# Optimization experiments

Measured on AMD Instinct MI355X. Metric: run time of the kernel, lower is better.

## Reference

```python
import jax, jax.numpy as jnp
import numpy as np

T, B, N, KALL, F, ORD, DIN, H, NH, HD, DE, DOUT = 4, 4, 16384, 4, 16384, 3, 4, 64, 4, 16, 4, 64


def setup_inputs() -> dict:
    key = jax.random.key(0)
    ks = jax.random.split(key, 32)
    p = lambda k, shape: (jax.random.normal(k, shape) * 0.1).astype(jnp.float32)
    indices = jax.random.randint(ks[0], (F, ORD), 0, N, dtype=jnp.int32)
    cnt = jnp.zeros((N,), jnp.float32).at[indices.reshape(-1)].add(1.0)
    nnz = jnp.maximum(cnt, 1.0)  # per-node nonzero count (avoid div-by-zero)
    return {
        "h": p(ks[1], (B, N, H)),
        "h_global": p(ks[2], (B, KALL, DOUT)),
        "x": p(ks[3], (T, B, N, DIN)),
        "extra": p(ks[4], (T, B, KALL, DE)),
        "dones": jax.random.bernoulli(ks[5], 0.1, (T, B)),
        "indices": indices,
        "nnz": nnz,
        # GRU cell params (flax GRUCell layout: i-dense with bias, h-dense no bias except n-gate)
        "Wi": p(ks[6], (DIN, 3 * H)), "bi": p(ks[7], (3 * H,)),
        "Wh": p(ks[8], (H, 3 * H)), "bhn": p(ks[9], (H,)),
        # MultiHeadAttention params
        "Wq": p(ks[10], (H, NH, HD)), "bq": p(ks[11], (NH, HD)),
        "Wk": p(ks[12], (H, NH, HD)), "bk": p(ks[13], (NH, HD)),
        "Wv": p(ks[14], (H, NH, HD)), "bv": p(ks[15], (NH, HD)),
        "Wo": p(ks[16], (NH, HD, H)), "bo": p(ks[17], (H,)),
        # output MLP (logit head) and value head
        "W1": p(ks[18], (H + DE, DOUT)), "b1": p(ks[19], (DOUT,)),
        "W2": p(ks[20], (DOUT, 1)), "b2": p(ks[21], (1,)),
        "Wv1": p(ks[22], (H + DE, 1)), "bv1": p(ks[23], (1,)),
    }


def reference(h, h_global, x, extra, dones, indices, nnz,
              Wi, bi, Wh, bhn, Wq, bq, Wk, bk, Wv, bv, Wo, bo,
              W1, b1, W2, b2, Wv1, bv1):
    Hd = Wh.shape[0]

    def gru_step(carry, inp):
        xt, dt = inp  # xt: [B,N,din], dt: [B]
        c = jnp.where(dt[:, None, None], jnp.zeros_like(carry), carry)
        gi = xt @ Wi + bi          # [B,N,3H]
        gh = c @ Wh                # [B,N,3H]
        r = jax.nn.sigmoid(gi[..., :Hd] + gh[..., :Hd])
        z = jax.nn.sigmoid(gi[..., Hd:2 * Hd] + gh[..., Hd:2 * Hd])
        n = jnp.tanh(gi[..., 2 * Hd:] + r * (gh[..., 2 * Hd:] + bhn))
        new = (1.0 - z) * n + z * c
        return new, new

    h_fin, hs = jax.lax.scan(gru_step, h, (x, dones))  # hs: [T,B,N,H]

    # gather per-factor neighbor hidden states
    g = jnp.take(hs, indices, axis=2)  # [T,B,F,ord,H]
    q = jnp.einsum('tbfkh,hnd->tbfknd', g, Wq) + bq
    kk = jnp.einsum('tbfkh,hnd->tbfknd', g, Wk) + bk
    vv = jnp.einsum('tbfkh,hnd->tbfknd', g, Wv) + bv
    scale = 1.0 / np.sqrt(q.shape[-1]).astype(np.float32)
    att = jax.nn.softmax(jnp.einsum('tbfqnd,tbfknd->tbfnqk', q * scale, kk), axis=-1)
    o = jnp.einsum('tbfnqk,tbfknd->tbfqnd', att, vv)
    a = jnp.einsum('tbfknd,ndh->tbfkh', o, Wo) + bo  # [T,B,F,ord,H]

    Tn, Bn = a.shape[0], a.shape[1]
    Nn = nnz.shape[0]
    a_flat = a.reshape(Tn, Bn, -1, a.shape[-1])  # [T,B,F*ord,H]
    # segment-sum scatter back to nodes, normalized by nnz
    y = jnp.zeros((Tn, Bn, Nn, a.shape[-1]), a.dtype).at[:, :, indices.reshape(-1), :].add(a_flat)
    y = y / nnz[None, None, :, None]

    Kall = extra.shape[2]
    N0 = Nn // Kall
    ypi = y.reshape(Tn, Bn, Kall, N0, y.shape[-1])
    y_global = jnp.mean(ypi, axis=3)                       # [T,B,K,H]
    z_global = jnp.concatenate((y_global, extra), axis=3)  # [T,B,K,H+DE]
    extra_t = jnp.broadcast_to(extra[:, :, :, None, :], (Tn, Bn, Kall, N0, extra.shape[-1]))
    z = jnp.concatenate((ypi, extra_t), axis=4).reshape(Tn, Bn, Nn, -1)
    value = (z_global @ Wv1 + bv1).sum(axis=2)             # [T,B,1]
    logit = (jax.nn.relu(z @ W1 + b1) @ W2 + b2).squeeze(axis=3)  # [T,B,N]
    return h_fin, h_global, logit, value.squeeze(axis=-1)
```

## Files before the change

kernel.cpp:

```cpp
#include <hip/hip_runtime.h>
#include <hip/hip_bf16.h>

#define T_ 4
#define B_ 4
#define N_ 16384
#define KALL_ 4
#define F_ 16384
#define ORD_ 3
#define DIN_ 4
#define H_ 64
#define H3_ 192
#define DE_ 4
#define STR 72
#define NE_ 49152

typedef __attribute__((ext_vector_type(8))) short s16x8;
typedef __attribute__((ext_vector_type(4))) float f32x4;
typedef unsigned long long u64;

static __device__ __forceinline__ float b2f(unsigned short u) {
  union { unsigned u; float f; } x; x.u = ((unsigned)u) << 16; return x.f;
}
static __device__ __forceinline__ unsigned short f2b(float f) {
  __hip_bfloat16 h = __float2bfloat16(f);
  union { __hip_bfloat16 h; unsigned short u; } x; x.h = h; return x.u;
}
static __device__ __forceinline__ float sigm_fast(float v) {
  return __builtin_amdgcn_rcpf(1.f + __expf(-v));
}
static __device__ __forceinline__ float tanh_fast(float v) {
  float e = __expf(2.f * v);
  return 1.f - 2.f * __builtin_amdgcn_rcpf(e + 1.f);
}

__global__ __launch_bounds__(256) void k_csr_count(
    const int* __restrict__ idx, int* __restrict__ cnt) {
  int e = blockIdx.x * 256 + threadIdx.x;
  if (e < NE_) atomicAdd(&cnt[idx[e]], 1);
}
__global__ __launch_bounds__(256) void k_csr_scan(
    const int* __restrict__ cnt, int* __restrict__ offs, int* __restrict__ cursor) {
  __shared__ int part[256];
  __shared__ int base[256];
  int t = threadIdx.x;
  int s = 0;
  for (int j = 0; j < 64; ++j) s += cnt[t * 64 + j];
  part[t] = s;
  __syncthreads();
  if (t == 0) {
    int run = 0;
    for (int i = 0; i < 256; ++i) { base[i] = run; run += part[i]; }
  }
  __syncthreads();
  int run = base[t];
  for (int j = 0; j < 64; ++j) {
    offs[t * 64 + j] = run;
    cursor[t * 64 + j] = run;
    run += cnt[t * 64 + j];
  }
  if (t == 255) offs[N_] = run;
}
__global__ __launch_bounds__(256) void k_csr_fill(
    const int* __restrict__ idx, int* __restrict__ cursor, int* __restrict__ elist) {
  int e = blockIdx.x * 256 + threadIdx.x;
  if (e < NE_) {
    int pos = atomicAdd(&cursor[idx[e]], 1);
    elist[pos] = e;
  }
}

__global__ __launch_bounds__(256) void k_prep_wh(
    const float* __restrict__ Wh, unsigned short* __restrict__ whTg) {
  int i = blockIdx.x * 256 + threadIdx.x;
  int rr = i >> 6, k = i & 63;
  int ct = rr >> 4, c = rr & 15;
  int g = ct >> 2, cg = ct & 3;
  whTg[i] = f2b(Wh[k * H3_ + g * 64 + 4 * c + cg]);
}

__global__ __launch_bounds__(256) void k_gru(
    const float* __restrict__ h0,
    const float* __restrict__ x,
    const int* __restrict__ dones,
    const unsigned short* __restrict__ whTg,
    const float* __restrict__ Wi,
    const float* __restrict__ bi,
    const float* __restrict__ bhn,
    unsigned short* __restrict__ hs,
    float* __restrict__ hfin)
{
  __shared__ __align__(16) short whT[H3_ * 72];
  __shared__ __align__(16) short carry[H_ * 72];
  __shared__ float wiS[5 * H3_];

  const int tid = threadIdx.x;
  const int lane = tid & 63;
  const int w = tid >> 6;
  const int c15 = lane & 15;
  const int hi4 = lane >> 4;
  const int bid = blockIdx.x;
  const int b = bid >> 8;
  const int nbase = (bid & 255) * 64;
  const int hb = 4 * c15;

#pragma unroll
  for (int c = 0; c < 6; ++c) {
    int lin = (c * 256 + tid) * 8;
    int row = lin >> 6, col = lin & 63;
    *(s16x8*)&whT[row * 72 + col] = *(const s16x8*)&whTg[lin];
  }
  for (int i = tid; i < 5 * H3_; i += 256)
    wiS[i] = (i < 4 * H3_) ? Wi[i] : bi[i - 4 * H3_];

  f32x4 cf[4];
#pragma unroll
  for (int r = 0; r < 4; ++r) {
    int row = 16 * w + 4 * hi4 + r;
    cf[r] = *(const f32x4*)&h0[(size_t)(b * N_ + nbase + row) * H_ + hb];
    u64 pk = 0;
#pragma unroll
    for (int e = 0; e < 4; ++e) pk |= (u64)f2b(cf[r][e]) << (16 * e);
    *(u64*)&carry[row * 72 + hb] = pk;
  }

  float bhnr[4];
#pragma unroll
  for (int cg = 0; cg < 4; ++cg) bhnr[cg] = bhn[hb + cg];

  unsigned dmask = 0;
  {
    bool word = true;
#pragma unroll
    for (int i = 0; i < 16; ++i) {
      int v = dones[i];
      if (v != 0 && v != 1 && v != 0x3F800000) word = false;
    }
#pragma unroll
    for (int t = 0; t < T_; ++t) {
      int tb = t * B_ + b;
      bool d = word ? (dones[tb] != 0) : (((const unsigned char*)dones)[tb] != 0);
      if (d) dmask |= (1u << t);
    }
  }

  __syncthreads();

  const int rowA = 16 * w + c15;
  for (int t = 0; t < T_; ++t) {
    if ((dmask >> t) & 1u) {
#pragma unroll
      for (int r = 0; r < 4; ++r) {
        cf[r] = (f32x4){0.f, 0.f, 0.f, 0.f};
        *(u64*)&carry[(16 * w + 4 * hi4 + r) * 72 + hb] = 0ull;
      }
    }

    f32x4 acc[12];
#pragma unroll
    for (int ct = 0; ct < 12; ++ct) acc[ct] = (f32x4){0.f, 0.f, 0.f, 0.f};
#pragma unroll
    for (int ks = 0; ks < 2; ++ks) {
      const int kb = ks * 32 + hi4 * 8;
      s16x8 af = *(const s16x8*)&carry[rowA * 72 + kb];
#pragma unroll
      for (int ct = 0; ct < 12; ++ct) {
        s16x8 bfr = *(const s16x8*)&whT[(16 * ct + c15) * 72 + kb];
        acc[ct] = __builtin_amdgcn_mfma_f32_16x16x32_bf16(af, bfr, acc[ct], 0, 0, 0);
      }
    }

#pragma unroll
    for (int r = 0; r < 4; ++r) {
      const int row = 16 * w + 4 * hi4 + r;
      const int node = nbase + row;
      const f32x4 xv = *(const f32x4*)&x[(size_t)((t * B_ + b) * N_ + node) * DIN_];
      f32x4 gi[3];
#pragma unroll
      for (int g = 0; g < 3; ++g) {
        f32x4 s = *(const f32x4*)&wiS[4 * H3_ + g * 64 + hb];
#pragma unroll
        for (int kk = 0; kk < 4; ++kk) {
          f32x4 wv = *(const f32x4*)&wiS[kk * H3_ + g * 64 + hb];
          s += xv[kk] * wv;
        }
        gi[g] = s;
      }
      f32x4 nc4;
      u64 pk = 0;
#pragma unroll
      for (int cg = 0; cg < 4; ++cg) {
        float rg = sigm_fast(gi[0][cg] + acc[cg][r]);
        float zg = sigm_fast(gi[1][cg] + acc[4 + cg][r]);
        float ng = tanh_fast(gi[2][cg] + rg * (acc[8 + cg][r] + bhnr[cg]));
        float nc = zg * (cf[r][cg] - ng) + ng;
        nc4[cg] = nc;
        pk |= (u64)f2b(nc) << (16 * cg);
      }
      cf[r] = nc4;
      *(u64*)&hs[(size_t)((t * B_ + b) * N_ + node) * H_ + hb] = pk;
      *(u64*)&carry[row * 72 + hb] = pk;
      if (t == T_ - 1)
        *(f32x4*)&hfin[(size_t)(b * N_ + node) * H_ + hb] = nc4;
    }
  }
}

__global__ __launch_bounds__(256, 3) void k_attn(
    const int tb0,
    const unsigned short* __restrict__ hs,
    const int* __restrict__ indices,
    const float* __restrict__ Wq, const float* __restrict__ bq,
    const float* __restrict__ Wk, const float* __restrict__ bk,
    const float* __restrict__ Wv, const float* __restrict__ bv,
    const float* __restrict__ Wo, const float* __restrict__ bo,
    unsigned short* __restrict__ a_edge)
{
  __shared__ __align__(16) unsigned short bufrag[3072];
  __shared__ __align__(8)  unsigned short qkvs[9792];
  __shared__ float biasf[4][64];
  __shared__ int idxs[48];

  const int tid = threadIdx.x;
  const int lane = tid & 63;
  const int w = tid >> 6;
  const int c15 = lane & 15;
  const int hi4 = lane >> 4;
  const int bid = blockIdx.x;
  const int col = 16 * w + c15;
  const int swz = (c15 ^ (hi4 << 2));

  if (tid < 48) idxs[tid] = indices[bid * 48 + tid];
  if (tid < 64) {
    biasf[0][tid] = bq[tid];
    biasf[1][tid] = bk[tid];
    biasf[2][tid] = bv[tid];
    biasf[3][tid] = bo[tid];
  }

  s16x8 wB[3][2], wB3[2];
#pragma unroll
  for (int m = 0; m < 3; ++m) {
    const float* Wm = (m == 0) ? Wq : (m == 1) ? Wk : Wv;
#pragma unroll
    for (int ks = 0; ks < 2; ++ks) {
      union { s16x8 v; short s[8]; } u;
#pragma unroll
      for (int j = 0; j < 8; ++j)
        u.s[j] = (short)f2b(Wm[(ks * 32 + hi4 * 8 + j) * 64 + col]);
      wB[m][ks] = u.v;
    }
  }
#pragma unroll
  for (int ks = 0; ks < 2; ++ks) {
    union { s16x8 v; short s[8]; } u;
#pragma unroll
    for (int j = 0; j < 8; ++j)
      u.s[j] = (short)f2b(Wo[(ks * 32 + hi4 * 8 + j) * 64 + col]);
    wB3[ks] = u.v;
  }
  __syncthreads();

  u64 pf[3];
#pragma unroll
  for (int k = 0; k < 3; ++k) {
    int idx = k * 256 + tid, row = idx >> 4, g = idx & 15;
    pf[k] = *(const u64*)&hs[((size_t)tb0 * N_ + idxs[row]) * H_ + g * 4];
  }

  for (int it = 0; it < 8; ++it) {
    __syncthreads();
#pragma unroll
    for (int k = 0; k < 3; ++k) {
      int idx = k * 256 + tid, row = idx >> 4, g = idx & 15;
      int rt = row >> 4, cr = row & 15;
      int ks = g >> 3, h5 = (g >> 1) & 3, j = (g & 1) * 4;
      int cr2 = cr ^ (h5 << 2);
      *(u64*)&bufrag[((rt * 2 + ks) << 9) + ((h5 * 16 + cr2) << 3) + j] = pf[k];
    }
    __syncthreads();

    s16x8 afr[3][2];
#pragma unroll
    for (int rt = 0; rt < 3; ++rt)
#pragma unroll
      for (int ks = 0; ks < 2; ++ks)
        afr[rt][ks] = *(const s16x8*)&bufrag[((rt * 2 + ks) << 9) + ((hi4 * 16 + swz) << 3)];
#pragma unroll
    for (int m = 0; m < 3; ++m) {
      float bias = biasf[m][col];
      float scl = (m == 0) ? 0.25f : 1.f;
#pragma unroll
      for (int rt = 0; rt < 3; ++rt) {
        f32x4 acc = (f32x4){0.f, 0.f, 0.f, 0.f};
        acc = __builtin_amdgcn_mfma_f32_16x16x32_bf16(afr[rt][0], wB[m][0], acc, 0, 0, 0);
        acc = __builtin_amdgcn_mfma_f32_16x16x32_bf16(afr[rt][1], wB[m][1], acc, 0, 0, 0);
#pragma unroll
        for (int r = 0; r < 4; ++r) {
          int row = 16 * rt + hi4 * 4 + r;
          qkvs[m * 3264 + row * 68 + col] = f2b((acc[r] + bias) * scl);
        }
      }
    }
    if (it < 7) {
      const size_t base = (size_t)(tb0 + it + 1) * N_;
#pragma unroll
      for (int k = 0; k < 3; ++k) {
        int idx = k * 256 + tid, row = idx >> 4, g = idx & 15;
        pf[k] = *(const u64*)&hs[(base + idxs[row]) * H_ + g * 4];
      }
    }
    __syncthreads();

    {
      int f = tid >> 4, head = (tid >> 2) & 3, dq = tid & 3;
      int colb = head * 16 + dq * 4;
      float qv[3][4], kv[3][4], vv[3][4];
#pragma unroll
      for (int qi = 0; qi < 3; ++qi) {
        int base = (3 * f + qi) * 68 + colb;
        u64 uq = *(const u64*)&qkvs[base];
        u64 uk = *(const u64*)&qkvs[3264 + base];
        u64 uv = *(const u64*)&qkvs[6528 + base];
#pragma unroll
        for (int e = 0; e < 4; ++e) {
          qv[qi][e] = b2f((unsigned short)(uq >> (16 * e)));
          kv[qi][e] = b2f((unsigned short)(uk >> (16 * e)));
          vv[qi][e] = b2f((unsigned short)(uv >> (16 * e)));
        }
      }
      float s[3][3];
#pragma unroll
      for (int qi = 0; qi < 3; ++qi)
#pragma unroll
        for (int ki = 0; ki < 3; ++ki) {
          float a = qv[qi][0] * kv[ki][0] + qv[qi][1] * kv[ki][1]
                  + qv[qi][2] * kv[ki][2] + qv[qi][3] * kv[ki][3];
          a += __shfl_xor(a, 1, 64);
          a += __shfl_xor(a, 2, 64);
          s[qi][ki] = a;
        }
      const int ks2 = colb >> 5, h5b = (colb >> 3) & 3, jb = colb & 7;
#pragma unroll
      for (int qi = 0; qi < 3; ++qi) {
        float mx = fmaxf(s[qi][0], fmaxf(s[qi][1], s[qi][2]));
        float e0 = __expf(s[qi][0] - mx), e1 = __expf(s[qi][1] - mx), e2 = __expf(s[qi][2] - mx);
        float inv = 1.f / (e0 + e1 + e2);
        e0 *= inv; e1 *= inv; e2 *= inv;
        int row = 3 * f + qi;
        int rt = row >> 4, cr2 = (row & 15) ^ (h5b << 2);
        u64 pack = 0;
#pragma unroll
        for (int e = 0; e < 4; ++e) {
          float o = e0 * vv[0][e] + e1 * vv[1][e] + e2 * vv[2][e];
          pack |= (u64)f2b(o) << (16 * e);
        }
        *(u64*)&bufrag[((rt * 2 + ks2) << 9) + ((h5b * 16 + cr2) << 3) + jb] = pack;
      }
    }
    __syncthreads();

    {
      const float bo_ = biasf[3][col];
      const size_t abase = (size_t)it * NE_ + (size_t)bid * 48;
#pragma unroll
      for (int rt = 0; rt < 3; ++rt) {
        s16x8 o0 = *(const s16x8*)&bufrag[((rt * 2 + 0) << 9) + ((hi4 * 16 + swz) << 3)];
        s16x8 o1 = *(const s16x8*)&bufrag[((rt * 2 + 1) << 9) + ((hi4 * 16 + swz) << 3)];
        f32x4 acc = (f32x4){0.f, 0.f, 0.f, 0.f};
        acc = __builtin_amdgcn_mfma_f32_16x16x32_bf16(o0, wB3[0], acc, 0, 0, 0);
        acc = __builtin_amdgcn_mfma_f32_16x16x32_bf16(o1, wB3[1], acc, 0, 0, 0);
#pragma unroll
        for (int r = 0; r < 4; ++r) {
          int row = 16 * rt + hi4 * 4 + r;
          a_edge[(abase + row) * H_ + col] = f2b(acc[r] + bo_);
        }
      }
    }
  }
}

__global__ __launch_bounds__(256) void k_head(
    const int tb0,
    const unsigned short* __restrict__ a_edge,
    const int* __restrict__ offs, const int* __restrict__ elist,
    const float* __restrict__ nnz,
    const float* __restrict__ extra,
    const float* __restrict__ W1, const float* __restrict__ b1,
    const float* __restrict__ W2, const float* __restrict__ b2,
    float* __restrict__ yg,
    float* __restrict__ logit)
{
  __shared__ short w1T[64 * STR];
  __shared__ short arow[64 * STR];
  __shared__ int offsS[65];
  __shared__ int eidS[512];
  __shared__ float hEx[64];
  __shared__ float w2s[64];
  __shared__ float red[4][64];

  const int tid = threadIdx.x;
  const int lane = tid & 63;
  const int w = tid >> 6;
  const int c15 = lane & 15;
  const int hi4 = lane >> 4;
  const int bid = blockIdx.x;
  const int ls = bid >> 8;
  const int tb = tb0 + ls;
  const int nbase = (bid & 255) * 64;
  const int kall = nbase >> 12;

  for (int i = tid; i < 4096; i += 256) {
    int k = i >> 6, colc = i & 63;
    w1T[colc * STR + k] = (short)f2b(W1[i]);
  }
  if (tid < 65) offsS[tid] = offs[nbase + tid];
  if (tid < 64) {
    float s = b1[tid];
#pragma unroll
    for (int e = 0; e < 4; ++e)
      s += extra[(tb * KALL_ + kall) * DE_ + e] * W1[(64 + e) * 64 + tid];
    hEx[tid] = s;
    w2s[tid] = W2[tid];
  }
  const int ebeg = offs[nbase];
  const int ecnt = offs[nbase + 64] - ebeg;
  const bool fast = (ecnt <= 512);
  if (tid == 0) eidS[0] = 0;
  if (fast) {
    for (int j = tid; j < ecnt; j += 256) eidS[j] = elist[ebeg + j];
  }
  __syncthreads();

  const size_t ebase = (size_t)ls * NE_;
  float accp = 0.f;
  if (fast) {
    for (int r = w; r < 64; r += 4) {
      const int beg = offsS[r] - ebeg, end = offsS[r + 1] - ebeg;
      float s = 0.f;
#pragma unroll
      for (int u = 0; u < 8; ++u) {
        int p = beg + u;
        bool valid = p < end;
        int pc = valid ? p : 0;
        float v = b2f(a_edge[(ebase + eidS[pc]) * H_ + lane]);
        s += valid ? v : 0.f;
      }
      for (int p = beg + 8; p < end; ++p)
        s += b2f(a_edge[(ebase + eidS[p]) * H_ + lane]);
      float val = s / fmaxf((float)(end - beg), 1.f);
      accp += val;
      arow[r * STR + lane] = (short)f2b(val);
    }
  } else {
    for (int r = w; r < 64; r += 4) {
      const int beg = offsS[r], end = offsS[r + 1];
      float s = 0.f;
      for (int p = beg; p < end; ++p)
        s += b2f(a_edge[(ebase + elist[p]) * H_ + lane]);
      float val = s / fmaxf((float)(end - beg), 1.f);
      accp += val;
      arow[r * STR + lane] = (short)f2b(val);
    }
  }
  red[w][lane] = accp;
  __syncthreads();

  f32x4 acc[4];
#pragma unroll
  for (int ct = 0; ct < 4; ++ct) acc[ct] = (f32x4){0.f, 0.f, 0.f, 0.f};
#pragma unroll
  for (int ks = 0; ks < 2; ++ks) {
    int kb = ks * 32 + hi4 * 8;
    s16x8 af = *(const s16x8*)&arow[(16 * w + c15) * STR + kb];
#pragma unroll
    for (int ct = 0; ct < 4; ++ct) {
      s16x8 bfr = *(const s16x8*)&w1T[(16 * ct + c15) * STR + kb];
      acc[ct] = __builtin_amdgcn_mfma_f32_16x16x32_bf16(af, bfr, acc[ct], 0, 0, 0);
    }
  }
  const float b2v = b2[0];
#pragma unroll
  for (int r = 0; r < 4; ++r) {
    float s = 0.f;
#pragma unroll
    for (int ct = 0; ct < 4; ++ct) {
      int colc = 16 * ct + c15;
      s += fmaxf(acc[ct][r] + hEx[colc], 0.f) * w2s[colc];
    }
    s += __shfl_xor(s, 1, 64);
    s += __shfl_xor(s, 2, 64);
    s += __shfl_xor(s, 4, 64);
    s += __shfl_xor(s, 8, 64);
    if (c15 == 0)
      logit[tb * N_ + nbase + 16 * w + hi4 * 4 + r] = s + b2v;
  }
  if (tid < 64) {
    float sv = red[0][tid] + red[1][tid] + red[2][tid] + red[3][tid];
    atomicAdd(&yg[(tb * KALL_ + kall) * H_ + tid], sv);
  }
}

__global__ __launch_bounds__(256) void k_final(
    const float* __restrict__ yg,
    const float* __restrict__ extra,
    const float* __restrict__ Wv1, const float* __restrict__ bv1,
    const float* __restrict__ hg_in,
    float* __restrict__ value_out,
    float* __restrict__ hg_out)
{
  const int tid = threadIdx.x;
  if (tid < 16) {
    const float bv = bv1[0];
    float v = 0.f;
    for (int kall = 0; kall < 4; ++kall) {
      float s = bv;
      for (int hh = 0; hh < 64; ++hh)
        s += (yg[(tid * KALL_ + kall) * H_ + hh] * (1.f / 4096.f)) * Wv1[hh];
      for (int e = 0; e < 4; ++e)
        s += extra[(tid * KALL_ + kall) * DE_ + e] * Wv1[64 + e];
      v += s;
    }
    value_out[tid] = v;
  }
  for (int i = tid; i < 1024; i += 256) hg_out[i] = hg_in[i];
}

extern "C" void kernel_launch(void* const* d_in, const int* in_sizes, int n_in,
                              void* d_out, int out_size, void* d_ws, size_t ws_size,
                              hipStream_t stream)
{
  (void)in_sizes; (void)n_in; (void)out_size; (void)ws_size;
  const float* h0    = (const float*)d_in[0];
  const float* hg    = (const float*)d_in[1];
  const float* x     = (const float*)d_in[2];
  const float* extra = (const float*)d_in[3];
  const int*   dn    = (const int*)d_in[4];
  const int*   idx   = (const int*)d_in[5];
  const float* nnz   = (const float*)d_in[6];
  const float* Wi    = (const float*)d_in[7];
  const float* bi    = (const float*)d_in[8];
  const float* Wh    = (const float*)d_in[9];
  const float* bhn   = (const float*)d_in[10];
  const float* Wq    = (const float*)d_in[11];
  const float* bq    = (const float*)d_in[12];
  const float* Wk    = (const float*)d_in[13];
  const float* bk    = (const float*)d_in[14];
  const float* Wv    = (const float*)d_in[15];
  const float* bv    = (const float*)d_in[16];
  const float* Wo    = (const float*)d_in[17];
  const float* bo    = (const float*)d_in[18];
  const float* W1    = (const float*)d_in[19];
  const float* b1    = (const float*)d_in[20];
  const float* W2    = (const float*)d_in[21];
  const float* b2    = (const float*)d_in[22];
  const float* Wv1   = (const float*)d_in[23];
  const float* bv1   = (const float*)d_in[24];

  float* out = (float*)d_out;
  float* out_hfin  = out;
  float* out_hg    = out + 4194304;
  float* out_logit = out + 4195328;
  float* out_value = out + 4457472;

  char* wsb = (char*)d_ws;
  float*          yg     = (float*)wsb;
  int*            cnt    = (int*)(wsb + 16384);
  int*            offs   = (int*)(wsb + 81920);
  int*            cursor = (int*)(wsb + 147584);
  int*            elist  = (int*)(wsb + 213120);
  unsigned short* whTg   = (unsigned short*)(wsb + 409728);
  unsigned short* hs     = (unsigned short*)(wsb + 524288);
  unsigned short* a_edge = (unsigned short*)(wsb + 34078720);

  hipMemsetAsync(wsb, 0, 81920, stream);
  k_csr_count<<<192, 256, 0, stream>>>(idx, cnt);
  k_csr_scan<<<1, 256, 0, stream>>>(cnt, offs, cursor);
  k_csr_fill<<<192, 256, 0, stream>>>(idx, cursor, elist);
  k_prep_wh<<<48, 256, 0, stream>>>(Wh, whTg);
  k_gru<<<1024, 256, 0, stream>>>(h0, x, dn, whTg, Wi, bi, bhn, hs, out_hfin);
  for (int half = 0; half < 2; ++half) {
    const int tb0 = half * 8;
    k_attn<<<1024, 256, 0, stream>>>(tb0, hs, idx, Wq, bq, Wk, bk, Wv, bv,
                                     Wo, bo, a_edge);
    k_head<<<2048, 256, 0, stream>>>(tb0, a_edge, offs, elist, nnz, extra,
                                     W1, b1, W2, b2, yg, out_logit);
  }
  k_final<<<1, 256, 0, stream>>>(yg, extra, Wv1, bv1, hg, out_value, out_hg);
}
```

Before: 330.8 us.

## Split attention over time slices, pretranspose attention weights, halve GRU accumulators

```diff
diff --git a/kernel.cpp b/kernel.cpp
--- a/kernel.cpp
+++ b/kernel.cpp
@@ -16,6 +16,7 @@
 
 typedef __attribute__((ext_vector_type(8))) short s16x8;
 typedef __attribute__((ext_vector_type(4))) float f32x4;
+typedef __attribute__((ext_vector_type(2))) float f32x2;
 typedef unsigned long long u64;
 
 static __device__ __forceinline__ float b2f(unsigned short u) {
@@ -76,6 +77,16 @@
   int ct = rr >> 4, c = rr & 15;
   int g = ct >> 2, cg = ct & 3;
   whTg[i] = f2b(Wh[k * H3_ + g * 64 + 4 * c + cg]);
+}
+
+__global__ __launch_bounds__(256) void k_prep_wa(
+    const float* __restrict__ Wq, const float* __restrict__ Wk,
+    const float* __restrict__ Wv, const float* __restrict__ Wo,
+    unsigned short* __restrict__ wT) {
+  int i = blockIdx.x * 256 + threadIdx.x;
+  int m = i >> 12, col = (i >> 6) & 63, k = i & 63;
+  const float* Wm = (m == 0) ? Wq : (m == 1) ? Wk : (m == 2) ? Wv : Wo;
+  wT[i] = f2b(Wm[k * 64 + col]);
 }
 
 __global__ __launch_bounds__(256) void k_gru(
@@ -155,17 +166,56 @@
       }
     }
 
-    f32x4 acc[12];
-#pragma unroll
-    for (int ct = 0; ct < 12; ++ct) acc[ct] = (f32x4){0.f, 0.f, 0.f, 0.f};
-#pragma unroll
-    for (int ks = 0; ks < 2; ++ks) {
-      const int kb = ks * 32 + hi4 * 8;
-      s16x8 af = *(const s16x8*)&carry[rowA * 72 + kb];
-#pragma unroll
-      for (int ct = 0; ct < 12; ++ct) {
-        s16x8 bfr = *(const s16x8*)&whT[(16 * ct + c15) * 72 + kb];
-        acc[ct] = __builtin_amdgcn_mfma_f32_16x16x32_bf16(af, bfr, acc[ct], 0, 0, 0);
+    s16x8 af0 = *(const s16x8*)&carry[rowA * 72 + hi4 * 8];
+    s16x8 af1 = *(const s16x8*)&carry[rowA * 72 + 32 + hi4 * 8];
+
+    f32x4 xv[4];
+#pragma unroll
+    for (int r = 0; r < 4; ++r) {
+      const int node = nbase + 16 * w + 4 * hi4 + r;
+      xv[r] = *(const f32x4*)&x[(size_t)((t * B_ + b) * N_ + node) * DIN_];
+    }
+
+#pragma unroll
+    for (int hh = 0; hh < 2; ++hh) {
+      f32x4 acc[6];
+#pragma unroll
+      for (int j = 0; j < 6; ++j) acc[j] = (f32x4){0.f, 0.f, 0.f, 0.f};
+#pragma unroll
+      for (int j = 0; j < 6; ++j) {
+        const int ct = (j >> 1) * 4 + 2 * hh + (j & 1);
+        acc[j] = __builtin_amdgcn_mfma_f32_16x16x32_bf16(
+            af0, *(const s16x8*)&whT[(16 * ct + c15) * 72 + hi4 * 8], acc[j], 0, 0, 0);
+      }
+#pragma unroll
+      for (int j = 0; j < 6; ++j) {
+        const int ct = (j >> 1) * 4 + 2 * hh + (j & 1);
+        acc[j] = __builtin_amdgcn_mfma_f32_16x16x32_bf16(
+            af1, *(const s16x8*)&whT[(16 * ct + c15) * 72 + 32 + hi4 * 8], acc[j], 0, 0, 0);
+      }
+      const int hb2 = hb + 2 * hh;
+#pragma unroll
+      for (int r = 0; r < 4; ++r) {
+        f32x2 gi[3];
+#pragma unroll
+        for (int g = 0; g < 3; ++g) {
+          f32x2 s = *(const f32x2*)&wiS[4 * H3_ + g * 64 + hb2];
+#pragma unroll
+          for (int kk = 0; kk < 4; ++kk) {
+            f32x2 wv = *(const f32x2*)&wiS[kk * H3_ + g * 64 + hb2];
+            s += xv[r][kk] * wv;
+          }
+          gi[g] = s;
+        }
+#pragma unroll
+        for (int c2 = 0; c2 < 2; ++c2) {
+          const int cg = 2 * hh + c2;
+          float rg = sigm_fast(gi[0][c2] + acc[c2][r]);
+          float zg = sigm_fast(gi[1][c2] + acc[2 + c2][r]);
+          float ng = tanh_fast(gi[2][c2] + rg * (acc[4 + c2][r] + bhnr[cg]));
+          float nc = zg * (cf[r][cg] - ng) + ng;
+          cf[r][cg] = nc;
+        }
       }
     }
 
@@ -173,46 +223,24 @@
     for (int r = 0; r < 4; ++r) {
       const int row = 16 * w + 4 * hi4 + r;
       const int node = nbase + row;
-      const f32x4 xv = *(const f32x4*)&x[(size_t)((t * B_ + b) * N_ + node) * DIN_];
-      f32x4 gi[3];
-#pragma unroll
-      for (int g = 0; g < 3; ++g) {
-        f32x4 s = *(const f32x4*)&wiS[4 * H3_ + g * 64 + hb];
-#pragma unroll
-        for (int kk = 0; kk < 4; ++kk) {
-          f32x4 wv = *(const f32x4*)&wiS[kk * H3_ + g * 64 + hb];
-          s += xv[kk] * wv;
-        }
-        gi[g] = s;
-      }
-      f32x4 nc4;
       u64 pk = 0;
 #pragma unroll
-      for (int cg = 0; cg < 4; ++cg) {
-        float rg = sigm_fast(gi[0][cg] + acc[cg][r]);
-        float zg = sigm_fast(gi[1][cg] + acc[4 + cg][r]);
-        float ng = tanh_fast(gi[2][cg] + rg * (acc[8 + cg][r] + bhnr[cg]));
-        float nc = zg * (cf[r][cg] - ng) + ng;
-        nc4[cg] = nc;
-        pk |= (u64)f2b(nc) << (16 * cg);
-      }
-      cf[r] = nc4;
+      for (int e = 0; e < 4; ++e) pk |= (u64)f2b(cf[r][e]) << (16 * e);
       *(u64*)&hs[(size_t)((t * B_ + b) * N_ + node) * H_ + hb] = pk;
       *(u64*)&carry[row * 72 + hb] = pk;
       if (t == T_ - 1)
-        *(f32x4*)&hfin[(size_t)(b * N_ + node) * H_ + hb] = nc4;
-    }
-  }
-}
-
-__global__ __launch_bounds__(256, 3) void k_attn(
+        *(f32x4*)&hfin[(size_t)(b * N_ + node) * H_ + hb] = cf[r];
+    }
+  }
+}
+
+__global__ __launch_bounds__(256) void k_attn(
     const int tb0,
     const unsigned short* __restrict__ hs,
     const int* __restrict__ indices,
-    const float* __restrict__ Wq, const float* __restrict__ bq,
-    const float* __restrict__ Wk, const float* __restrict__ bk,
-    const float* __restrict__ Wv, const float* __restrict__ bv,
-    const float* __restrict__ Wo, const float* __restrict__ bo,
+    const unsigned short* __restrict__ wT,
+    const float* __restrict__ bq, const float* __restrict__ bk,
+    const float* __restrict__ bv, const float* __restrict__ bo,
     unsigned short* __restrict__ a_edge)
 {
   __shared__ __align__(16) unsigned short bufrag[3072];
@@ -226,10 +254,12 @@
   const int c15 = lane & 15;
   const int hi4 = lane >> 4;
   const int bid = blockIdx.x;
+  const int slice = bid >> 10;
+  const int fch = bid & 1023;
   const int col = 16 * w + c15;
   const int swz = (c15 ^ (hi4 << 2));
 
-  if (tid < 48) idxs[tid] = indices[bid * 48 + tid];
+  if (tid < 48) idxs[tid] = indices[fch * 48 + tid];
   if (tid < 64) {
     biasf[0][tid] = bq[tid];
     biasf[1][tid] = bk[tid];
@@ -239,141 +269,118 @@
 
   s16x8 wB[3][2], wB3[2];
 #pragma unroll
-  for (int m = 0; m < 3; ++m) {
-    const float* Wm = (m == 0) ? Wq : (m == 1) ? Wk : Wv;
-#pragma unroll
-    for (int ks = 0; ks < 2; ++ks) {
-      union { s16x8 v; short s[8]; } u;
-#pragma unroll
-      for (int j = 0; j < 8; ++j)
-        u.s[j] = (short)f2b(Wm[(ks * 32 + hi4 * 8 + j) * 64 + col]);
-      wB[m][ks] = u.v;
-    }
-  }
-#pragma unroll
-  for (int ks = 0; ks < 2; ++ks) {
-    union { s16x8 v; short s[8]; } u;
-#pragma unroll
-    for (int j = 0; j < 8; ++j)
-      u.s[j] = (short)f2b(Wo[(ks * 32 + hi4 * 8 + j) * 64 + col]);
-    wB3[ks] = u.v;
-  }
-  __syncthreads();
-
+  for (int m = 0; m < 3; ++m)
+#pragma unroll
+    for (int ks = 0; ks < 2; ++ks)
+      wB[m][ks] = *(const s16x8*)&wT[(m * 64 + col) * 64 + ks * 32 + hi4 * 8];
+#pragma unroll
+  for (int ks = 0; ks < 2; ++ks)
+    wB3[ks] = *(const s16x8*)&wT[(3 * 64 + col) * 64 + ks * 32 + hi4 * 8];
+  __syncthreads();
+
+  const size_t hbase = (size_t)(tb0 + slice) * N_;
   u64 pf[3];
 #pragma unroll
   for (int k = 0; k < 3; ++k) {
     int idx = k * 256 + tid, row = idx >> 4, g = idx & 15;
-    pf[k] = *(const u64*)&hs[((size_t)tb0 * N_ + idxs[row]) * H_ + g * 4];
-  }
-
-  for (int it = 0; it < 8; ++it) {
-    __syncthreads();
-#pragma unroll
-    for (int k = 0; k < 3; ++k) {
-      int idx = k * 256 + tid, row = idx >> 4, g = idx & 15;
-      int rt = row >> 4, cr = row & 15;
-      int ks = g >> 3, h5 = (g >> 1) & 3, j = (g & 1) * 4;
-      int cr2 = cr ^ (h5 << 2);
-      *(u64*)&bufrag[((rt * 2 + ks) << 9) + ((h5 * 16 + cr2) << 3) + j] = pf[k];
-    }
-    __syncthreads();
-
-    s16x8 afr[3][2];
-#pragma unroll
-    for (int rt = 0; rt < 3; ++rt)
-#pragma unroll
-      for (int ks = 0; ks < 2; ++ks)
-        afr[rt][ks] = *(const s16x8*)&bufrag[((rt * 2 + ks) << 9) + ((hi4 * 16 + swz) << 3)];
-#pragma unroll
-    for (int m = 0; m < 3; ++m) {
-      float bias = biasf[m][col];
-      float scl = (m == 0) ? 0.25f : 1.f;
-#pragma unroll
-      for (int rt = 0; rt < 3; ++rt) {
-        f32x4 acc = (f32x4){0.f, 0.f, 0.f, 0.f};
-        acc = __builtin_amdgcn_mfma_f32_16x16x32_bf16(afr[rt][0], wB[m][0], acc, 0, 0, 0);
-        acc = __builtin_amdgcn_mfma_f32_16x16x32_bf16(afr[rt][1], wB[m][1], acc, 0, 0, 0);
-#pragma unroll
-        for (int r = 0; r < 4; ++r) {
-          int row = 16 * rt + hi4 * 4 + r;
-          qkvs[m * 3264 + row * 68 + col] = f2b((acc[r] + bias) * scl);
-        }
-      }
-    }
-    if (it < 7) {
-      const size_t base = (size_t)(tb0 + it + 1) * N_;
-#pragma unroll
-      for (int k = 0; k < 3; ++k) {
-        int idx = k * 256 + tid, row = idx >> 4, g = idx & 15;
-        pf[k] = *(const u64*)&hs[(base + idxs[row]) * H_ + g * 4];
-      }
-    }
-    __syncthreads();
-
-    {
-      int f = tid >> 4, head = (tid >> 2) & 3, dq = tid & 3;
-      int colb = head * 16 + dq * 4;
-      float qv[3][4], kv[3][4], vv[3][4];
-#pragma unroll
-      for (int qi = 0; qi < 3; ++qi) {
-        int base = (3 * f + qi) * 68 + colb;
-        u64 uq = *(const u64*)&qkvs[base];
-        u64 uk = *(const u64*)&qkvs[3264 + base];
-        u64 uv = *(const u64*)&qkvs[6528 + base];
-#pragma unroll
-        for (int e = 0; e < 4; ++e) {
-          qv[qi][e] = b2f((unsigned short)(uq >> (16 * e)));
-          kv[qi][e] = b2f((unsigned short)(uk >> (16 * e)));
-          vv[qi][e] = b2f((unsigned short)(uv >> (16 * e)));
-        }
-      }
-      float s[3][3];
-#pragma unroll
-      for (int qi = 0; qi < 3; ++qi)
-#pragma unroll
-        for (int ki = 0; ki < 3; ++ki) {
-          float a = qv[qi][0] * kv[ki][0] + qv[qi][1] * kv[ki][1]
-                  + qv[qi][2] * kv[ki][2] + qv[qi][3] * kv[ki][3];
-          a += __shfl_xor(a, 1, 64);
-          a += __shfl_xor(a, 2, 64);
-          s[qi][ki] = a;
-        }
-      const int ks2 = colb >> 5, h5b = (colb >> 3) & 3, jb = colb & 7;
-#pragma unroll
-      for (int qi = 0; qi < 3; ++qi) {
-        float mx = fmaxf(s[qi][0], fmaxf(s[qi][1], s[qi][2]));
-        float e0 = __expf(s[qi][0] - mx), e1 = __expf(s[qi][1] - mx), e2 = __expf(s[qi][2] - mx);
-        float inv = 1.f / (e0 + e1 + e2);
-        e0 *= inv; e1 *= inv; e2 *= inv;
-        int row = 3 * f + qi;
-        int rt = row >> 4, cr2 = (row & 15) ^ (h5b << 2);
-        u64 pack = 0;
-#pragma unroll
-        for (int e = 0; e < 4; ++e) {
-          float o = e0 * vv[0][e] + e1 * vv[1][e] + e2 * vv[2][e];
-          pack |= (u64)f2b(o) << (16 * e);
-        }
-        *(u64*)&bufrag[((rt * 2 + ks2) << 9) + ((h5b * 16 + cr2) << 3) + jb] = pack;
-      }
-    }
-    __syncthreads();
-
-    {
-      const float bo_ = biasf[3][col];
-      const size_t abase = (size_t)it * NE_ + (size_t)bid * 48;
-#pragma unroll
-      for (int rt = 0; rt < 3; ++rt) {
-        s16x8 o0 = *(const s16x8*)&bufrag[((rt * 2 + 0) << 9) + ((hi4 * 16 + swz) << 3)];
-        s16x8 o1 = *(const s16x8*)&bufrag[((rt * 2 + 1) << 9) + ((hi4 * 16 + swz) << 3)];
-        f32x4 acc = (f32x4){0.f, 0.f, 0.f, 0.f};
-        acc = __builtin_amdgcn_mfma_f32_16x16x32_bf16(o0, wB3[0], acc, 0, 0, 0);
-        acc = __builtin_amdgcn_mfma_f32_16x16x32_bf16(o1, wB3[1], acc, 0, 0, 0);
-#pragma unroll
-        for (int r = 0; r < 4; ++r) {
-          int row = 16 * rt + hi4 * 4 + r;
-          a_edge[(abase + row) * H_ + col] = f2b(acc[r] + bo_);
-        }
+    pf[k] = *(const u64*)&hs[(hbase + idxs[row]) * H_ + g * 4];
+  }
+#pragma unroll
+  for (int k = 0; k < 3; ++k) {
+    int idx = k * 256 + tid, row = idx >> 4, g = idx & 15;
+    int rt = row >> 4, cr = row & 15;
+    int ks = g >> 3, h5 = (g >> 1) & 3, j = (g & 1) * 4;
+    int cr2 = cr ^ (h5 << 2);
+    *(u64*)&bufrag[((rt * 2 + ks) << 9) + ((h5 * 16 + cr2) << 3) + j] = pf[k];
+  }
+  __syncthreads();
+
+  s16x8 afr[3][2];
+#pragma unroll
+  for (int rt = 0; rt < 3; ++rt)
+#pragma unroll
+    for (int ks = 0; ks < 2; ++ks)
+      afr[rt][ks] = *(const s16x8*)&bufrag[((rt * 2 + ks) << 9) + ((hi4 * 16 + swz) << 3)];
+#pragma unroll
+  for (int m = 0; m < 3; ++m) {
+    float bias = biasf[m][col];
+    float scl = (m == 0) ? 0.25f : 1.f;
+#pragma unroll
+    for (int rt = 0; rt < 3; ++rt) {
+      f32x4 acc = (f32x4){0.f, 0.f, 0.f, 0.f};
+      acc = __builtin_amdgcn_mfma_f32_16x16x32_bf16(afr[rt][0], wB[m][0], acc, 0, 0, 0);
+      acc = __builtin_amdgcn_mfma_f32_16x16x32_bf16(afr[rt][1], wB[m][1], acc, 0, 0, 0);
+#pragma unroll
+      for (int r = 0; r < 4; ++r) {
+        int row = 16 * rt + hi4 * 4 + r;
+        qkvs[m * 3264 + row * 68 + col] = f2b((acc[r] + bias) * scl);
+      }
+    }
+  }
+  __syncthreads();
+
+  {
+    int f = tid >> 4, head = (tid >> 2) & 3, dq = tid & 3;
+    int colb = head * 16 + dq * 4;
+    float qv[3][4], kv[3][4], vv[3][4];
+#pragma unroll
+    for (int qi = 0; qi < 3; ++qi) {
+      int base = (3 * f + qi) * 68 + colb;
+      u64 uq = *(const u64*)&qkvs[base];
+      u64 uk = *(const u64*)&qkvs[3264 + base];
+      u64 uv = *(const u64*)&qkvs[6528 + base];
+#pragma unroll
+      for (int e = 0; e < 4; ++e) {
+        qv[qi][e] = b2f((unsigned short)(uq >> (16 * e)));
+        kv[qi][e] = b2f((unsigned short)(uk >> (16 * e)));
+        vv[qi][e] = b2f((unsigned short)(uv >> (16 * e)));
+      }
+    }
+    float s[3][3];
+#pragma unroll
+    for (int qi = 0; qi < 3; ++qi)
+#pragma unroll
+      for (int ki = 0; ki < 3; ++ki) {
+        float a = qv[qi][0] * kv[ki][0] + qv[qi][1] * kv[ki][1]
+                + qv[qi][2] * kv[ki][2] + qv[qi][3] * kv[ki][3];
+        a += __shfl_xor(a, 1, 64);
+        a += __shfl_xor(a, 2, 64);
+        s[qi][ki] = a;
+      }
+    const int ks2 = colb >> 5, h5b = (colb >> 3) & 3, jb = colb & 7;
+#pragma unroll
+    for (int qi = 0; qi < 3; ++qi) {
+      float mx = fmaxf(s[qi][0], fmaxf(s[qi][1], s[qi][2]));
+      float e0 = __expf(s[qi][0] - mx), e1 = __expf(s[qi][1] - mx), e2 = __expf(s[qi][2] - mx);
+      float inv = 1.f / (e0 + e1 + e2);
+      e0 *= inv; e1 *= inv; e2 *= inv;
+      int row = 3 * f + qi;
+      int rt = row >> 4, cr2 = (row & 15) ^ (h5b << 2);
+      u64 pack = 0;
+#pragma unroll
+      for (int e = 0; e < 4; ++e) {
+        float o = e0 * vv[0][e] + e1 * vv[1][e] + e2 * vv[2][e];
+        pack |= (u64)f2b(o) << (16 * e);
+      }
+      *(u64*)&bufrag[((rt * 2 + ks2) << 9) + ((h5b * 16 + cr2) << 3) + jb] = pack;
+    }
+  }
+  __syncthreads();
+
+  {
+    const float bo_ = biasf[3][col];
+    const size_t abase = (size_t)slice * NE_ + (size_t)fch * 48;
+#pragma unroll
+    for (int rt = 0; rt < 3; ++rt) {
+      s16x8 o0 = *(const s16x8*)&bufrag[((rt * 2 + 0) << 9) + ((hi4 * 16 + swz) << 3)];
+      s16x8 o1 = *(const s16x8*)&bufrag[((rt * 2 + 1) << 9) + ((hi4 * 16 + swz) << 3)];
+      f32x4 acc = (f32x4){0.f, 0.f, 0.f, 0.f};
+      acc = __builtin_amdgcn_mfma_f32_16x16x32_bf16(o0, wB3[0], acc, 0, 0, 0);
+      acc = __builtin_amdgcn_mfma_f32_16x16x32_bf16(o1, wB3[1], acc, 0, 0, 0);
+#pragma unroll
+      for (int r = 0; r < 4; ++r) {
+        int row = 16 * rt + hi4 * 4 + r;
+        a_edge[(abase + row) * H_ + col] = f2b(acc[r] + bo_);
       }
     }
   }
@@ -569,6 +576,7 @@
   int*            cursor = (int*)(wsb + 147584);
   int*            elist  = (int*)(wsb + 213120);
   unsigned short* whTg   = (unsigned short*)(wsb + 409728);
+  unsigned short* wT     = (unsigned short*)(wsb + 434304);
   unsigned short* hs     = (unsigned short*)(wsb + 524288);
   unsigned short* a_edge = (unsigned short*)(wsb + 34078720);
 
@@ -577,11 +585,11 @@
   k_csr_scan<<<1, 256, 0, stream>>>(cnt, offs, cursor);
   k_csr_fill<<<192, 256, 0, stream>>>(idx, cursor, elist);
   k_prep_wh<<<48, 256, 0, stream>>>(Wh, whTg);
+  k_prep_wa<<<64, 256, 0, stream>>>(Wq, Wk, Wv, Wo, wT);
   k_gru<<<1024, 256, 0, stream>>>(h0, x, dn, whTg, Wi, bi, bhn, hs, out_hfin);
   for (int half = 0; half < 2; ++half) {
     const int tb0 = half * 8;
-    k_attn<<<1024, 256, 0, stream>>>(tb0, hs, idx, Wq, bq, Wk, bk, Wv, bv,
-                                     Wo, bo, a_edge);
+    k_attn<<<8192, 256, 0, stream>>>(tb0, hs, idx, wT, bq, bk, bv, bo, a_edge);
     k_head<<<2048, 256, 0, stream>>>(tb0, a_edge, offs, elist, nnz, extra,
                                      W1, b1, W2, b2, yg, out_logit);
   }
```

Measured after the change: 338.4 us. 2.3% more time.
